# Performance work log

Hardware: AMD Instinct MI355X
Metric: run time of the kernel (lower is better)

## Reference

```python
import jax, jax.numpy as jnp
import numpy as np

NUM_CLASSES = 80
IMG = 608.0
L_COORD, L_NOOBJ, L_CLS = 5.0, 0.5, 1.0
EPS = 1e-7
ANCHORS = jnp.array([[12,16],[19,36],[40,28],[36,75],[76,55],[72,146],
                     [142,110],[192,243],[459,401]], dtype=jnp.float32).reshape(3, 3, 2)


def _iou(b1, b2):
    # boxes in (cx, cy, w, h); broadcastable shapes [..., 4]
    b1x1 = b1[..., 0] - b1[..., 2] * 0.5; b1y1 = b1[..., 1] - b1[..., 3] * 0.5
    b1x2 = b1[..., 0] + b1[..., 2] * 0.5; b1y2 = b1[..., 1] + b1[..., 3] * 0.5
    b2x1 = b2[..., 0] - b2[..., 2] * 0.5; b2y1 = b2[..., 1] - b2[..., 3] * 0.5
    b2x2 = b2[..., 0] + b2[..., 2] * 0.5; b2y2 = b2[..., 1] + b2[..., 3] * 0.5
    iw = jnp.clip(jnp.minimum(b1x2, b2x2) - jnp.maximum(b1x1, b2x1), 0.0)
    ih = jnp.clip(jnp.minimum(b1y2, b2y2) - jnp.maximum(b1y1, b2y1), 0.0)
    inter = iw * ih
    union = (b1x2 - b1x1) * (b1y2 - b1y1) + (b2x2 - b2x1) * (b2y2 - b2y1) - inter + EPS
    return inter / union


def _scale_loss(pred, anchors, targets):
    # pred: [B, A, H, W, 5+C]; anchors: [A, 2] (pixels); targets: [B, T, 5+C]
    B, A, H, W, _ = pred.shape
    C = pred.shape[-1] - 5
    T = targets.shape[1]

    # ---- decode predictions (decodePredictionsStable) ----
    gy, gx = jnp.meshgrid(jnp.arange(H), jnp.arange(W), indexing='ij')
    grid = jnp.stack([gx, gy], axis=-1).astype(pred.dtype)          # [H, W, 2]
    xy = jax.nn.sigmoid(pred[..., :2])
    wh = jnp.clip(pred[..., 2:4], -10.0, 10.0)
    box_xy = jnp.clip((xy + grid) / jnp.array([W, H], dtype=pred.dtype), 0.0, 1.0)
    box_wh = jnp.clip(jnp.exp(wh) * anchors[None, :, None, None, :] / IMG, 0.0, 1.0)
    pbox = jnp.concatenate([box_xy, box_wh], axis=-1)               # [B,A,H,W,4]
    pconf = jax.nn.sigmoid(pred[..., 4])                            # [B,A,H,W]
    pcls = jax.nn.sigmoid(pred[..., 5:])                            # [B,A,H,W,C]

    # ---- build targets (buildTargetsStable, vectorized scatter) ----
    gtbox = jnp.clip(targets[..., :4], 0.0, 1.0)                    # [B,T,4]
    valid = targets[..., 4] > 0                                     # [B,T]
    gxi = jnp.clip((gtbox[..., 0] * W).astype(jnp.int32), 0, W - 1)
    gyi = jnp.clip((gtbox[..., 1] * H).astype(jnp.int32), 0, H - 1)
    abox = jnp.concatenate([jnp.full((A, 2), 0.5, dtype=pred.dtype), anchors / IMG], axis=-1)
    ious = _iou(abox[None, None, :, :], gtbox[:, :, None, :])       # [B,T,A]
    best = jnp.argmax(ious, axis=-1).astype(jnp.int32)              # first max == torch strict '>' loop
    bidx = jnp.broadcast_to(jnp.arange(B, dtype=jnp.int32)[:, None], (B, T))

    flat = ((bidx * A + best) * H + gyi) * W + gxi                  # [B,T]
    order = jnp.arange(B * T, dtype=jnp.int32).reshape(B, T)
    ncells = B * A * H * W
    winner = jnp.full((ncells,), -1, jnp.int32).at[jnp.where(valid, flat, ncells)].max(order, mode='drop')
    keep = valid & (winner[flat] == order)
    bw = jnp.where(keep, bidx, B)                                   # out-of-range -> dropped

    mask = jnp.zeros((B, A, H, W), pred.dtype).at[bw, best, gyi, gxi].set(1.0, mode='drop')
    tbox = jnp.zeros((B, A, H, W, 4), pred.dtype).at[bw, best, gyi, gxi].set(gtbox, mode='drop')
    tcls = jnp.zeros((B, A, H, W, C), pred.dtype).at[bw, best, gyi, gxi].set(targets[..., 5:5 + C], mode='drop')

    npos = jnp.sum(mask)
    nneg = jnp.asarray(mask.size, pred.dtype) - npos

    # ---- coordinate loss: mean(1 - IoU) over positives ----
    coord = jnp.where(npos > 0, jnp.sum((1.0 - _iou(pbox, tbox)) * mask) / jnp.maximum(npos, 1.0), 0.0)

    # ---- confidence loss: BCE sum/npos + lambdaNoObj * BCE sum/nneg ----
    p = jnp.clip(pconf, 1e-10, 1.0 - 1e-10)
    bce = -(mask * jnp.log(p) + (1.0 - mask) * jnp.log1p(-p))
    conf = jnp.sum(bce * mask) / jnp.maximum(npos, 1.0) \
         + L_NOOBJ * jnp.sum(bce * (1.0 - mask)) / jnp.maximum(nneg, 1.0)

    # ---- class loss: BCE mean over positive rows ----
    pc = jnp.clip(pcls, 1e-10, 1.0 - 1e-10)
    tc = jnp.clip(tcls, 0.0, 1.0)
    bcec = -(tc * jnp.log(pc) + (1.0 - tc) * jnp.log1p(-pc))
    cls = jnp.where(npos > 0, jnp.sum(bcec * mask[..., None]) / jnp.maximum(npos * C, 1.0), 0.0)

    return coord, conf, cls


def setup_inputs() -> dict:
    key = jax.random.key(0)
    k0, k1, k2, k3 = jax.random.split(key, 4)
    B, T, C = 16, 50, NUM_CLASSES
    pred0 = jax.random.normal(k0, (B, 3, 76, 76, 5 + C), dtype=jnp.float32)
    pred1 = jax.random.normal(k1, (B, 3, 38, 38, 5 + C), dtype=jnp.float32)
    pred2 = jax.random.normal(k2, (B, 3, 19, 19, 5 + C), dtype=jnp.float32)
    targets = jax.random.uniform(k3, (B, T, 5 + C), dtype=jnp.float32)
    return {"pred0": pred0, "pred1": pred1, "pred2": pred2, "targets": targets}


def reference(pred0, pred1, pred2, targets):
    coord = jnp.float32(0.0); conf = jnp.float32(0.0); cls = jnp.float32(0.0)
    for s, pred in enumerate((pred0, pred1, pred2)):
        c, cf, cl = _scale_loss(pred, ANCHORS[s], targets)
        coord = coord + c; conf = conf + cf; cls = cls + cl
    total = L_COORD * coord + conf + L_CLS * cls
    return total, coord, conf, cls
```

## Files before the change

kernel.cpp:

```cpp
#include <hip/hip_runtime.h>
#include <math.h>

#define BB   16
#define TT   50
#define BT   (BB*TT)
#define NCLS 80
#define IMGF 608.0f

#define H0 76
#define H1 38
#define H2 19
#define N0 277248
#define N1 69312
#define N2 17328
#define NTOT (N0+N1+N2)

#define NB0 1083
#define NB1 271
#define NB2 68
#define NBNO (NB0+NB1+NB2)
#define POS_BLOCKS_PER_SCALE 200
#define NPOS_BLOCKS (3*POS_BLOCKS_PER_SCALE)

__constant__ float c_anchors[3][3][2] = {
    {{12.f,16.f},{19.f,36.f},{40.f,28.f}},
    {{36.f,75.f},{76.f,55.f},{72.f,146.f}},
    {{142.f,110.f},{192.f,243.f},{459.f,401.f}}};
__constant__ int c_H[3]        = {H0, H1, H2};
__constant__ int c_cell_off[3] = {0, N0, N0 + N1};

__device__ __forceinline__ float sigmoidf_(float x) { return 1.0f / (1.0f + expf(-x)); }
__device__ __forceinline__ float clipf_(float x, float lo, float hi) {
    return fminf(fmaxf(x, lo), hi);
}

__device__ __forceinline__ float iou4(float ax, float ay, float aw, float ah,
                                      float bx, float by, float bw, float bh) {
    float ax1 = ax - aw * 0.5f, ay1 = ay - ah * 0.5f;
    float ax2 = ax + aw * 0.5f, ay2 = ay + ah * 0.5f;
    float bx1 = bx - bw * 0.5f, by1 = by - bh * 0.5f;
    float bx2 = bx + bw * 0.5f, by2 = by + bh * 0.5f;
    float iw = fmaxf(fminf(ax2, bx2) - fmaxf(ax1, bx1), 0.f);
    float ih = fmaxf(fminf(ay2, by2) - fmaxf(ay1, by1), 0.f);
    float inter = iw * ih;
    float uni = (ax2 - ax1) * (ay2 - ay1) + (bx2 - bx1) * (by2 - by1) - inter + 1e-7f;
    return inter / uni;
}

__device__ __forceinline__ int target_cell(const float* tr, int s, float& cx, float& cy,
                                           float& w, float& h, int& best, int& gxi, int& gyi) {
    float t4 = tr[4];
    if (!(t4 > 0.f)) return -1;
    cx = clipf_(tr[0], 0.f, 1.f);
    cy = clipf_(tr[1], 0.f, 1.f);
    w  = clipf_(tr[2], 0.f, 1.f);
    h  = clipf_(tr[3], 0.f, 1.f);
    best = 0;
    float bi = -1e30f;
    #pragma unroll
    for (int a = 0; a < 3; a++) {
        float aw = c_anchors[s][a][0] / IMGF;
        float ah = c_anchors[s][a][1] / IMGF;
        float v = iou4(0.5f, 0.5f, aw, ah, cx, cy, w, h);
        if (v > bi) { bi = v; best = a; }
    }
    int H = c_H[s];
    gxi = (int)(cx * (float)H); gxi = min(max(gxi, 0), H - 1);
    gyi = (int)(cy * (float)H); gyi = min(max(gyi, 0), H - 1);
    return 0;
}

__global__ __launch_bounds__(256) void k_targets(const float* __restrict__ targets,
                                                 int* __restrict__ winner) {
    int idx = blockIdx.x * 256 + threadIdx.x;
    if (idx >= 3 * BT) return;
    int s = idx / BT;
    int order = idx % BT;
    const float* tr = targets + order * 85;
    float cx, cy, w, h; int best, gxi, gyi;
    if (target_cell(tr, s, cx, cy, w, h, best, gxi, gyi) < 0) return;
    int H = c_H[s];
    int b = order / TT;
    int flat = ((b * 3 + best) * H + gyi) * H + gxi;
    atomicMax(&winner[c_cell_off[s] + flat], order);
}

__global__ __launch_bounds__(256) void k_main(const float* __restrict__ p0,
                                              const float* __restrict__ p1,
                                              const float* __restrict__ p2,
                                              const float* __restrict__ targets,
                                              const int* __restrict__ winner,
                                              float* __restrict__ noobj_part,
                                              float* __restrict__ pos_part) {
    int blk = blockIdx.x;
    int lane = threadIdx.x & 63;
    int wv = threadIdx.x >> 6;

    if (blk < NBNO) {
        const float* pred; int base, n;
        if (blk < NB0)            { pred = p0; base = 0;         n = N0; }
        else if (blk < NB0 + NB1) { pred = p1; base = NB0;       n = N1; }
        else                      { pred = p2; base = NB0 + NB1; n = N2; }
        int c = (blk - base) * 256 + threadIdx.x;
        float v = 0.f;
        if (c < n) {
            float p = clipf_(sigmoidf_(pred[c * 85 + 4]), 1e-10f, 1.0f);
            v = -log1pf(-p);
        }
        #pragma unroll
        for (int off = 32; off > 0; off >>= 1) v += __shfl_xor(v, off, 64);
        __shared__ float sm[4];
        if (lane == 0) sm[wv] = v;
        __syncthreads();
        if (threadIdx.x == 0) noobj_part[blk] = sm[0] + sm[1] + sm[2] + sm[3];
    } else {
        int bp = blk - NBNO;
        int s = bp / POS_BLOCKS_PER_SCALE;
        int order = (bp % POS_BLOCKS_PER_SCALE) * 4 + wv;

        float v_coord = 0.f, v_obj = 0.f, v_noadj = 0.f, v_cls = 0.f, v_np = 0.f;

        const float* tr = targets + order * 85;
        float cx, cy, w, h; int best, gxi, gyi;
        if (target_cell(tr, s, cx, cy, w, h, best, gxi, gyi) == 0) {
            int H = c_H[s];
            int b = order / TT;
            int flat = ((b * 3 + best) * H + gyi) * H + gxi;
            if (winner[c_cell_off[s] + flat] == order) {
                const float* pred = (s == 0) ? p0 : (s == 1) ? p1 : p2;
                const float* pc = pred + (long long)flat * 85;

                float px = sigmoidf_(pc[0]);
                float py = sigmoidf_(pc[1]);
                float bx = clipf_((px + (float)gxi) / (float)H, 0.f, 1.f);
                float by = clipf_((py + (float)gyi) / (float)H, 0.f, 1.f);
                float aw = c_anchors[s][best][0], ah = c_anchors[s][best][1];
                float bwv = clipf_(expf(clipf_(pc[2], -10.f, 10.f)) * aw / IMGF, 0.f, 1.f);
                float bhv = clipf_(expf(clipf_(pc[3], -10.f, 10.f)) * ah / IMGF, 0.f, 1.f);
                float iou = iou4(bx, by, bwv, bhv, cx, cy, w, h);

                float p = clipf_(sigmoidf_(pc[4]), 1e-10f, 1.0f);

                float pcv = clipf_(sigmoidf_(pc[5 + lane]), 1e-10f, 1.0f);
                float tc  = clipf_(tr[5 + lane], 0.f, 1.f);
                float cl  = -(tc * logf(pcv) + (1.f - tc) * log1pf(-pcv));
                if (lane < NCLS - 64) {
                    float pcv2 = clipf_(sigmoidf_(pc[5 + 64 + lane]), 1e-10f, 1.0f);
                    float tc2  = clipf_(tr[5 + 64 + lane], 0.f, 1.f);
                    cl += -(tc2 * logf(pcv2) + (1.f - tc2) * log1pf(-pcv2));
                }
                #pragma unroll
                for (int off = 32; off > 0; off >>= 1) cl += __shfl_xor(cl, off, 64);

                v_coord = 1.f - iou;
                v_obj   = -logf(p);
                v_noadj = -log1pf(-p);
                v_cls   = cl;
                v_np    = 1.f;
            }
        }

        __shared__ float psum[4][5];
        if (lane == 0) {
            psum[wv][0] = v_coord; psum[wv][1] = v_obj; psum[wv][2] = v_noadj;
            psum[wv][3] = v_cls;   psum[wv][4] = v_np;
        }
        __syncthreads();
        if (threadIdx.x < 5) {
            pos_part[bp * 5 + threadIdx.x] =
                psum[0][threadIdx.x] + psum[1][threadIdx.x] +
                psum[2][threadIdx.x] + psum[3][threadIdx.x];
        }
    }
}

__global__ __launch_bounds__(256) void k_final(const float* __restrict__ noobj_part,
                                               const float* __restrict__ pos_part,
                                               float* __restrict__ out) {
    float nsum[3] = {0.f, 0.f, 0.f};
    for (int i = threadIdx.x; i < NBNO; i += 256) {
        float v = noobj_part[i];
        if (i < NB0)            nsum[0] += v;
        else if (i < NB0 + NB1) nsum[1] += v;
        else                    nsum[2] += v;
    }
    float ps[3][5] = {};
    for (int i = threadIdx.x; i < NPOS_BLOCKS; i += 256) {
        int s = i / POS_BLOCKS_PER_SCALE;
        #pragma unroll
        for (int q = 0; q < 5; q++) ps[s][q] += pos_part[i * 5 + q];
    }

    __shared__ float red[18][256];
    #pragma unroll
    for (int s = 0; s < 3; s++) {
        red[s][threadIdx.x] = nsum[s];
        #pragma unroll
        for (int q = 0; q < 5; q++) red[3 + s * 5 + q][threadIdx.x] = ps[s][q];
    }
    __syncthreads();
    for (int off = 128; off > 0; off >>= 1) {
        if (threadIdx.x < off) {
            #pragma unroll
            for (int r = 0; r < 18; r++)
                red[r][threadIdx.x] += red[r][threadIdx.x + off];
        }
        __syncthreads();
    }
    if (threadIdx.x == 0) {
        const float ncell[3] = {(float)N0, (float)N1, (float)N2};
        float coord = 0.f, conf = 0.f, cls = 0.f;
        #pragma unroll
        for (int s = 0; s < 3; s++) {
            float noobjTot = red[s][0];
            float co   = red[3 + s * 5 + 0][0];
            float ob   = red[3 + s * 5 + 1][0];
            float noadj= red[3 + s * 5 + 2][0];
            float cl   = red[3 + s * 5 + 3][0];
            float npos = red[3 + s * 5 + 4][0];
            float nneg = ncell[s] - npos;
            float dn = fmaxf(npos, 1.f);
            conf += ob / dn + 0.5f * (noobjTot - noadj) / fmaxf(nneg, 1.f);
            if (npos > 0.f) {
                coord += co / dn;
                cls   += cl / fmaxf(npos * (float)NCLS, 1.f);
            }
        }
        out[0] = 5.0f * coord + conf + 1.0f * cls;
        out[1] = coord;
        out[2] = conf;
        out[3] = cls;
    }
}

extern "C" void kernel_launch(void* const* d_in, const int* in_sizes, int n_in,
                              void* d_out, int out_size, void* d_ws, size_t ws_size,
                              hipStream_t stream) {
    const float* p0 = (const float*)d_in[0];
    const float* p1 = (const float*)d_in[1];
    const float* p2 = (const float*)d_in[2];
    const float* tg = (const float*)d_in[3];
    float* out = (float*)d_out;

    char* ws = (char*)d_ws;
    int* winner = (int*)ws;
    float* noobj_part = (float*)(ws + (size_t)NTOT * 4);
    float* pos_part = (float*)(ws + (size_t)NTOT * 4 + NBNO * 4 + 64);

    hipMemsetAsync(winner, 0xFF, (size_t)NTOT * 4, stream);
    k_targets<<<(3 * BT + 255) / 256, 256, 0, stream>>>(tg, winner);
    k_main<<<NBNO + NPOS_BLOCKS, 256, 0, stream>>>(p0, p1, p2, tg, winner,
                                                   noobj_part, pos_part);
    k_final<<<1, 256, 0, stream>>>(noobj_part, pos_part, out);
}
```

Measured before the change: 163.3 us.

## Replace winner-table scatter with in-wave later-target collision check

Removes the memset of a per-cell winner table and the atomicMax targets kernel. Each wave instead checks, one lane per later target in the same image, whether any of them maps to the same cell, and uses a ballot to decide whether this target is the last writer. This drops a large memset and one kernel launch. In exchange every positive wave redoes up to 49 target-cell computations.

```diff
diff --git a/kernel.cpp b/kernel.cpp
--- a/kernel.cpp
+++ b/kernel.cpp
@@ -26,8 +26,7 @@
     {{12.f,16.f},{19.f,36.f},{40.f,28.f}},
     {{36.f,75.f},{76.f,55.f},{72.f,146.f}},
     {{142.f,110.f},{192.f,243.f},{459.f,401.f}}};
-__constant__ int c_H[3]        = {H0, H1, H2};
-__constant__ int c_cell_off[3] = {0, N0, N0 + N1};
+__constant__ int c_H[3] = {H0, H1, H2};
 
 __device__ __forceinline__ float sigmoidf_(float x) { return 1.0f / (1.0f + expf(-x)); }
 __device__ __forceinline__ float clipf_(float x, float lo, float hi) {
@@ -70,26 +69,10 @@
     return 0;
 }
 
-__global__ __launch_bounds__(256) void k_targets(const float* __restrict__ targets,
-                                                 int* __restrict__ winner) {
-    int idx = blockIdx.x * 256 + threadIdx.x;
-    if (idx >= 3 * BT) return;
-    int s = idx / BT;
-    int order = idx % BT;
-    const float* tr = targets + order * 85;
-    float cx, cy, w, h; int best, gxi, gyi;
-    if (target_cell(tr, s, cx, cy, w, h, best, gxi, gyi) < 0) return;
-    int H = c_H[s];
-    int b = order / TT;
-    int flat = ((b * 3 + best) * H + gyi) * H + gxi;
-    atomicMax(&winner[c_cell_off[s] + flat], order);
-}
-
 __global__ __launch_bounds__(256) void k_main(const float* __restrict__ p0,
                                               const float* __restrict__ p1,
                                               const float* __restrict__ p2,
                                               const float* __restrict__ targets,
-                                              const int* __restrict__ winner,
                                               float* __restrict__ noobj_part,
                                               float* __restrict__ pos_part) {
     int blk = blockIdx.x;
@@ -120,13 +103,24 @@
 
         float v_coord = 0.f, v_obj = 0.f, v_noadj = 0.f, v_cls = 0.f, v_np = 0.f;
 
+        int b = order / TT, t = order % TT;
         const float* tr = targets + order * 85;
         float cx, cy, w, h; int best, gxi, gyi;
         if (target_cell(tr, s, cx, cy, w, h, best, gxi, gyi) == 0) {
             int H = c_H[s];
-            int b = order / TT;
             int flat = ((b * 3 + best) * H + gyi) * H + gxi;
-            if (winner[c_cell_off[s] + flat] == order) {
+
+            bool lost = false;
+            int tp = t + 1 + lane;
+            if (tp < TT) {
+                const float* tr2 = targets + (b * TT + tp) * 85;
+                float cx2, cy2, w2, h2; int best2, gxi2, gyi2;
+                if (target_cell(tr2, s, cx2, cy2, w2, h2, best2, gxi2, gyi2) == 0) {
+                    int flat2 = ((b * 3 + best2) * H + gyi2) * H + gxi2;
+                    lost = (flat2 == flat);
+                }
+            }
+            if (__ballot(lost) == 0ull) {
                 const float* pred = (s == 0) ? p0 : (s == 1) ? p1 : p2;
                 const float* pc = pred + (long long)flat * 85;
 
@@ -213,11 +207,11 @@
         #pragma unroll
         for (int s = 0; s < 3; s++) {
             float noobjTot = red[s][0];
-            float co   = red[3 + s * 5 + 0][0];
-            float ob   = red[3 + s * 5 + 1][0];
-            float noadj= red[3 + s * 5 + 2][0];
-            float cl   = red[3 + s * 5 + 3][0];
-            float npos = red[3 + s * 5 + 4][0];
+            float co    = red[3 + s * 5 + 0][0];
+            float ob    = red[3 + s * 5 + 1][0];
+            float noadj = red[3 + s * 5 + 2][0];
+            float cl    = red[3 + s * 5 + 3][0];
+            float npos  = red[3 + s * 5 + 4][0];
             float nneg = ncell[s] - npos;
             float dn = fmaxf(npos, 1.f);
             conf += ob / dn + 0.5f * (noobjTot - noadj) / fmaxf(nneg, 1.f);
@@ -243,13 +237,10 @@
     float* out = (float*)d_out;
 
     char* ws = (char*)d_ws;
-    int* winner = (int*)ws;
-    float* noobj_part = (float*)(ws + (size_t)NTOT * 4);
-    float* pos_part = (float*)(ws + (size_t)NTOT * 4 + NBNO * 4 + 64);
-
-    hipMemsetAsync(winner, 0xFF, (size_t)NTOT * 4, stream);
-    k_targets<<<(3 * BT + 255) / 256, 256, 0, stream>>>(tg, winner);
-    k_main<<<NBNO + NPOS_BLOCKS, 256, 0, stream>>>(p0, p1, p2, tg, winner,
+    float* noobj_part = (float*)ws;
+    float* pos_part = (float*)(ws + 8192);
+
+    k_main<<<NBNO + NPOS_BLOCKS, 256, 0, stream>>>(p0, p1, p2, tg,
                                                    noobj_part, pos_part);
     k_final<<<1, 256, 0, stream>>>(noobj_part, pos_part, out);
 }
```

Result: faster. 158.6 us (-2.9%).
